# Kernel optimization log

Measured on AMD Instinct MI355X. Metric: run time of the kernel, lower is better.

The kernel has to match this reference:

```python
import jax, jax.numpy as jnp
import numpy as np

B, T, TC, C, CC, H = 2, 2048, 512, 1024, 512, 16
D = C // H  # head dim = 64


def setup_inputs() -> dict:
    key = jax.random.key(0)
    ks = jax.random.split(key, 18)
    w = lambda k, i, o: (jax.random.normal(k, (i, o), jnp.float32) / np.sqrt(i).astype(np.float32))
    return {
        "x": jax.random.normal(ks[0], (B, T, C), jnp.float32),
        "cross_input": jax.random.normal(ks[1], (B, TC, CC), jnp.float32),
        "Wk": w(ks[2], C, C),  "bk": jnp.zeros((C,), jnp.float32),
        "Wq": w(ks[3], C, C),  "bq": jnp.zeros((C,), jnp.float32),
        "Wv": w(ks[4], C, C),  "bv": jnp.zeros((C,), jnp.float32),
        "Wck": w(ks[5], CC, C), "bck": jnp.zeros((C,), jnp.float32),
        "Wcq": w(ks[6], C, C),  "bcq": jnp.zeros((C,), jnp.float32),
        "Wcv": w(ks[7], CC, C), "bcv": jnp.zeros((C,), jnp.float32),
        "Wp": w(ks[8], C, C),   "bp": jnp.zeros((C,), jnp.float32),
    }


def _heads(t):
    # [B, L, C] -> [B, H, L, D]
    b, l, _ = t.shape
    return t.reshape(b, l, H, D).transpose(0, 2, 1, 3)


def reference(x, cross_input, Wk, bk, Wq, bq, Wv, bv, Wck, bck, Wcq, bcq, Wcv, bcv, Wp, bp):
    scale = np.float32(1.0 / np.sqrt(D))
    q = _heads(x @ Wq + bq)
    k = _heads(x @ Wk + bk)
    v = _heads(x @ Wv + bv)
    # causal self-attention with materialized scores (faithful to original)
    att = jnp.einsum("bhqd,bhkd->bhqk", q, k) * scale
    causal = jnp.tril(jnp.ones((T, T), bool))
    att = jnp.where(causal[None, None], att, -jnp.inf)
    y = jnp.einsum("bhqk,bhkd->bhqd", jax.nn.softmax(att, axis=-1), v)
    # cross-attention (no mask)
    qc = _heads(x @ Wcq + bcq)
    kc = _heads(cross_input @ Wck + bck)
    vc = _heads(cross_input @ Wcv + bcv)
    attc = jnp.einsum("bhqd,bhkd->bhqk", qc, kc) * scale
    y = y + jnp.einsum("bhqk,bhkd->bhqd", jax.nn.softmax(attc, axis=-1), vc)
    # merge heads + output projection (dropout prob = 0 -> identity)
    y = y.transpose(0, 2, 1, 3).reshape(x.shape[0], T, C)
    return y @ Wp + bp
```

## Files before the change

### kernel.cpp

```cpp
#include <hip/hip_runtime.h>
#include <hip/hip_bf16.h>
#include <type_traits>

typedef __bf16 bf16;
typedef __bf16 bf16x8 __attribute__((ext_vector_type(8)));
typedef float floatx4 __attribute__((ext_vector_type(4)));
typedef unsigned int uint32x4 __attribute__((ext_vector_type(4)));

#if __has_builtin(__builtin_amdgcn_exp2f)
#define EXP2(x) __builtin_amdgcn_exp2f(x)
#else
#define EXP2(x) exp2f(x)
#endif

__device__ __forceinline__ void glds16(const bf16* g, bf16* l) {
  __builtin_amdgcn_global_load_lds((const __attribute__((address_space(1))) void*)g,
                                   (__attribute__((address_space(3))) void*)l, 16, 0, 0);
}

__device__ __forceinline__ unsigned pack_bf16(float a, float b) {
  unsigned short ua = __builtin_bit_cast(unsigned short, (bf16)a);
  unsigned short ub = __builtin_bit_cast(unsigned short, (bf16)b);
  return (unsigned)ua | ((unsigned)ub << 16);
}

struct PrepArgs {
  const float* x; const float* xc;
  bf16* xbf; bf16* xcbf;
  const float* b4[4];
  const float* bc[2];
  float* bias4; float* biasc;
  const float* W[7];
  bf16* WT[7];
};

__global__ __launch_bounds__(256) void prep_kernel(PrepArgs a) {
  __shared__ bf16 tsh[32][33];
  const int bx = blockIdx.x, tid = threadIdx.x;
  if (bx < 4096) {
    int i = bx * 256 + tid;
    float4 f = ((const float4*)a.x)[i];
    bf16 t[4] = {(bf16)f.x, (bf16)f.y, (bf16)f.z, (bf16)f.w};
    *(uint2*)&a.xbf[(long)i * 4] = *(const uint2*)t;
  } else if (bx < 4608) {
    int i = (bx - 4096) * 256 + tid;
    float4 f = ((const float4*)a.xc)[i];
    bf16 t[4] = {(bf16)f.x, (bf16)f.y, (bf16)f.z, (bf16)f.w};
    *(uint2*)&a.xcbf[(long)i * 4] = *(const uint2*)t;
  } else if (bx < 4632) {
    int lb = bx - 4608;
    if (lb < 16) {
      int i = lb * 256 + tid;
      int sec = i >> 10;
      float v = a.b4[sec][i & 1023];
      if (sec == 0 || sec == 3) v *= 0.18033688f;
      a.bias4[i] = v;
    } else {
      int i = (lb - 16) * 256 + tid;
      a.biasc[i] = a.bc[i >> 10][i & 1023];
    }
  } else {
    int t = bx - 4632, w, R, bxw, byw;
    if (t < 5120) { w = t >> 10; R = 1024; int l = t & 1023; bxw = l & 31; byw = l >> 5; }
    else { int t2 = t - 5120; w = 5 + (t2 >> 9); R = 512; int l = t2 & 511; bxw = l & 31; byw = l >> 5; }
    const float* in = a.W[w];
    bf16* out = a.WT[w];
    const float sc = (w == 0 || w == 3) ? 0.18033688f : 1.0f;
    int tx = tid & 31, ty = tid >> 5;
    int c = bxw * 32 + tx;
#pragma unroll
    for (int i = 0; i < 4; i++) {
      int r = byw * 32 + ty + i * 8;
      tsh[ty + i * 8][tx] = (bf16)(in[(long)r * 1024 + c] * sc);
    }
    __syncthreads();
    int oc = byw * 32 + tx;
#pragma unroll
    for (int i = 0; i < 4; i++) {
      int orr = bxw * 32 + ty + i * 8;
      out[(long)orr * R + oc] = tsh[tx][ty + i * 8];
    }
  }
}

template <typename OutT>
__global__ __launch_bounds__(256, 3) void gemm128(const bf16* __restrict__ A,
                                                  const bf16* __restrict__ Bt,
                                                  const float* __restrict__ bias,
                                                  OutT* __restrict__ C,
                                                  int M, int N, int K, int ldc,
                                                  bf16* __restrict__ Vt,
                                                  int vcol0, int vcol1, int Lt, int tok_shift) {
  __shared__ alignas(16) bf16 As[128 * 32];
  __shared__ alignas(16) bf16 Bs[128 * 32];
  const int tid = threadIdx.x, wave = tid >> 6, lane = tid & 63;
  const int l16 = lane & 15, l4 = lane >> 4;
  const int wm = wave & 1, wn = wave >> 1;
  const int n0 = blockIdx.x * 128, m0 = blockIdx.y * 128;
  const int lrow = lane >> 2, lch = (lane & 3) * 8;

  floatx4 acc[4][4];
#pragma unroll
  for (int mt = 0; mt < 4; mt++)
#pragma unroll
    for (int nt = 0; nt < 4; nt++) acc[mt][nt] = (floatx4){0.f, 0.f, 0.f, 0.f};

  const bf16* Ag = A + (long)(m0 + wave * 32 + lrow) * K + lch;
  const bf16* Bg = Bt + (long)(n0 + wave * 32 + lrow) * K + lch;
  bf16* Al = &As[(wave * 32) * 32];
  bf16* Bl = &Bs[(wave * 32) * 32];

  for (int k0 = 0; k0 < K; k0 += 32) {
    __syncthreads();
    glds16(Ag + k0, Al);
    glds16(Ag + k0 + (long)16 * K, Al + 16 * 32);
    glds16(Bg + k0, Bl);
    glds16(Bg + k0 + (long)16 * K, Bl + 16 * 32);
    __syncthreads();
    bf16x8 a[4], b[4];
#pragma unroll
    for (int mt = 0; mt < 4; mt++) a[mt] = *(const bf16x8*)&As[(wm * 64 + mt * 16 + l16) * 32 + l4 * 8];
#pragma unroll
    for (int nt = 0; nt < 4; nt++) b[nt] = *(const bf16x8*)&Bs[(wn * 64 + nt * 16 + l16) * 32 + l4 * 8];
#pragma unroll
    for (int mt = 0; mt < 4; mt++)
#pragma unroll
      for (int nt = 0; nt < 4; nt++)
        acc[mt][nt] = __builtin_amdgcn_mfma_f32_16x16x32_bf16(a[mt], b[nt], acc[mt][nt], 0, 0, 0);
  }

  const bool vpath = (vcol0 >= 0) && (n0 >= vcol0) && (n0 < vcol1);
  if (!vpath) {
    const int coladj = (vcol0 >= 0 && n0 >= vcol1) ? (vcol1 - vcol0) : 0;
#pragma unroll
    for (int nt = 0; nt < 4; nt++) {
      int col = n0 + wn * 64 + nt * 16 + l16;
      float bv = bias[col];
#pragma unroll
      for (int mt = 0; mt < 4; mt++)
#pragma unroll
        for (int r = 0; r < 4; r++) {
          int row = m0 + wm * 64 + mt * 16 + l4 * 4 + r;
          float v = acc[mt][nt][r] + bv;
          if constexpr (std::is_same_v<OutT, float>) C[(long)row * ldc + col - coladj] = v;
          else                                       C[(long)row * ldc + col - coladj] = (bf16)v;
        }
    }
  } else {
#pragma unroll
    for (int nt = 0; nt < 4; nt++) {
      int col = n0 + wn * 64 + nt * 16 + l16;
      int c = col - vcol0, hh = c >> 6, dd = c & 63;
      float bv = bias[col];
#pragma unroll
      for (int mt = 0; mt < 4; mt++) {
        int t0 = m0 + wm * 64 + mt * 16 + l4 * 4;
        int bb = t0 >> tok_shift, t = t0 & ((1 << tok_shift) - 1);
        t = (t & ~31) | (((t >> 2) & 3) << 3) | (((t >> 4) & 1) << 2) | (t & 3);
        bf16 tmp[4];
#pragma unroll
        for (int r = 0; r < 4; r++) tmp[r] = (bf16)(acc[mt][nt][r] + bv);
        *(uint2*)&Vt[(((long)bb * 16 + hh) * 64 + dd) * Lt + t] = *(const uint2*)tmp;
      }
    }
  }
}

__global__ __launch_bounds__(256, 2) void attn_kernel(const bf16* __restrict__ QKQc,
                                                      const bf16* __restrict__ VtB,
                                                      const bf16* __restrict__ KcB,
                                                      const bf16* __restrict__ VctB,
                                                      bf16* __restrict__ Y) {
  __shared__ float Lbuf[4][4][16];
  __shared__ alignas(16) bf16 U[4 * 64 * 72];
  const int tid = threadIdx.x, w = tid >> 6, lane = tid & 63;
  const int l16 = lane & 15, l4 = lane >> 4;
  const int bh = blockIdx.x, h = bh & 15, b = bh >> 4;
  const int qt = 31 - (int)blockIdx.y;
  const int q0 = qt * 64;
  const int wk = w * 32;
  const float NEG = -1e30f;

  float o_self[16];

  for (int phase = 0; phase < 2; phase++) {
    const bf16 *Qb, *Kb, *Vtb;
    int kstr, vtstr, nkt;
    if (phase == 0) {
      Qb = QKQc + (long)b * 2048 * 3072 + h * 64;
      Kb = Qb + 1024;                              kstr = 3072;
      Vtb = VtB + ((long)b * 16 + h) * 64 * 2048;  vtstr = 2048;
      nkt = (qt + 2) >> 1;
    } else {
      Qb = QKQc + (long)b * 2048 * 3072 + h * 64 + 2048;
      Kb = KcB + (long)b * 512 * 1024 + h * 64;    kstr = 1024;
      Vtb = VctB + ((long)b * 16 + h) * 64 * 512;  vtstr = 512;
      nkt = 4;
    }

    __syncthreads();

    bf16x8 qf[4][2];
#pragma unroll
    for (int qtt = 0; qtt < 4; qtt++) {
      const bf16* qp = Qb + (long)(q0 + qtt * 16 + l16) * 3072 + l4 * 8;
#pragma unroll
      for (int ds = 0; ds < 2; ds++) qf[qtt][ds] = *(const bf16x8*)(qp + ds * 32);
    }

    float l_i[4];
#pragma unroll
    for (int qtt = 0; qtt < 4; qtt++) l_i[qtt] = 0.f;
    floatx4 oacc[4][4];
#pragma unroll
    for (int mtd = 0; mtd < 4; mtd++)
#pragma unroll
      for (int qtt = 0; qtt < 4; qtt++) oacc[mtd][qtt] = (floatx4){0.f, 0.f, 0.f, 0.f};

    bf16x8 kreg[2][2];
#pragma unroll
    for (int mt = 0; mt < 2; mt++)
#pragma unroll
      for (int ds = 0; ds < 2; ds++)
        kreg[mt][ds] = *(const bf16x8*)(Kb + (long)(wk + mt * 16 + l16) * kstr + ds * 32 + l4 * 8);

    floatx4 sacc[2][4];
#pragma unroll
    for (int mt = 0; mt < 2; mt++)
#pragma unroll
      for (int qtt = 0; qtt < 4; qtt++) sacc[mt][qtt] = (floatx4){0.f, 0.f, 0.f, 0.f};
#pragma unroll
    for (int ds = 0; ds < 2; ds++)
#pragma unroll
      for (int mt = 0; mt < 2; mt++)
#pragma unroll
        for (int qtt = 0; qtt < 4; qtt++)
          sacc[mt][qtt] = __builtin_amdgcn_mfma_f32_16x16x32_bf16(kreg[mt][ds], qf[qtt][ds], sacc[mt][qtt], 0, 0, 0);

    for (int kt = 0; kt < nkt; kt++) {
      const int kbase = kt * 128 + wk;
      const bool more = (kt + 1 < nkt);

      bf16x8 vc[4];
#pragma unroll
      for (int mtd = 0; mtd < 4; mtd++)
        vc[mtd] = *(const bf16x8*)(Vtb + (long)(mtd * 16 + l16) * vtstr + kbase + l4 * 8);

      if (more) {
        const int nb = kbase + 128;
#pragma unroll
        for (int mt = 0; mt < 2; mt++)
#pragma unroll
          for (int ds = 0; ds < 2; ds++)
            kreg[mt][ds] = *(const bf16x8*)(Kb + (long)(nb + mt * 16 + l16) * kstr + ds * 32 + l4 * 8);
      }

      if (phase == 0 && kt == nkt - 1) {
#pragma unroll
        for (int mt = 0; mt < 2; mt++) {
          int keyb = kbase + mt * 16 + l4 * 4;
#pragma unroll
          for (int qtt = 0; qtt < 4; qtt++) {
            int q = q0 + qtt * 16 + l16;
#pragma unroll
            for (int r = 0; r < 4; r++)
              if (keyb + r > q) sacc[mt][qtt][r] = NEG;
          }
        }
      }

#pragma unroll
      for (int qtt = 0; qtt < 4; qtt++) {
        float p0 = EXP2(sacc[0][qtt][0]), p1 = EXP2(sacc[0][qtt][1]);
        float p2 = EXP2(sacc[0][qtt][2]), p3 = EXP2(sacc[0][qtt][3]);
        float p4 = EXP2(sacc[1][qtt][0]), p5 = EXP2(sacc[1][qtt][1]);
        float p6 = EXP2(sacc[1][qtt][2]), p7 = EXP2(sacc[1][qtt][3]);
        l_i[qtt] += ((p0 + p1) + (p2 + p3)) + ((p4 + p5) + (p6 + p7));
        uint32x4 pu = {pack_bf16(p0, p1), pack_bf16(p2, p3), pack_bf16(p4, p5), pack_bf16(p6, p7)};
        bf16x8 pf = __builtin_bit_cast(bf16x8, pu);
        __builtin_amdgcn_s_setprio(1);
#pragma unroll
        for (int mtd = 0; mtd < 4; mtd++)
          oacc[mtd][qtt] = __builtin_amdgcn_mfma_f32_16x16x32_bf16(vc[mtd], pf, oacc[mtd][qtt], 0, 0, 0);
        __builtin_amdgcn_s_setprio(0);
      }

      if (more) {
#pragma unroll
        for (int mt = 0; mt < 2; mt++)
#pragma unroll
          for (int qtt = 0; qtt < 4; qtt++) sacc[mt][qtt] = (floatx4){0.f, 0.f, 0.f, 0.f};
        __builtin_amdgcn_s_setprio(1);
#pragma unroll
        for (int ds = 0; ds < 2; ds++)
#pragma unroll
          for (int mt = 0; mt < 2; mt++)
#pragma unroll
            for (int qtt = 0; qtt < 4; qtt++)
              sacc[mt][qtt] = __builtin_amdgcn_mfma_f32_16x16x32_bf16(kreg[mt][ds], qf[qtt][ds], sacc[mt][qtt], 0, 0, 0);
        __builtin_amdgcn_s_setprio(0);
      }
    }

    float lsum[4];
#pragma unroll
    for (int qtt = 0; qtt < 4; qtt++) {
      float r = l_i[qtt];
      r += __shfl_xor(r, 16);
      r += __shfl_xor(r, 32);
      lsum[qtt] = r;
    }
    if (l4 == 0) {
#pragma unroll
      for (int qtt = 0; qtt < 4; qtt++) Lbuf[w][qtt][l16] = lsum[qtt];
    }
    __syncthreads();
    float denom[4];
#pragma unroll
    for (int qtt = 0; qtt < 4; qtt++)
      denom[qtt] = Lbuf[0][qtt][l16] + Lbuf[1][qtt][l16] + Lbuf[2][qtt][l16] + Lbuf[3][qtt][l16];
#pragma unroll
    for (int qtt = 0; qtt < 4; qtt++)
#pragma unroll
      for (int mtd = 0; mtd < 4; mtd++) {
        uint2 u = {pack_bf16(oacc[mtd][qtt][0], oacc[mtd][qtt][1]),
                   pack_bf16(oacc[mtd][qtt][2], oacc[mtd][qtt][3])};
        *(uint2*)&U[((w * 64) + qtt * 16 + l16) * 72 + mtd * 16 + l4 * 4] = u;
      }
    __syncthreads();
    float sum[16];
#pragma unroll
    for (int j = 0; j < 16; j++) sum[j] = 0.f;
#pragma unroll
    for (int s = 0; s < 4; s++) {
      bf16x8 c0 = *(const bf16x8*)&U[((s * 64) + w * 16 + l16) * 72 + l4 * 16];
      bf16x8 c1 = *(const bf16x8*)&U[((s * 64) + w * 16 + l16) * 72 + l4 * 16 + 8];
#pragma unroll
      for (int j = 0; j < 8; j++) { sum[j] += (float)c0[j]; sum[8 + j] += (float)c1[j]; }
    }
    float invd = 1.0f / denom[w];
    if (phase == 0) {
#pragma unroll
      for (int j = 0; j < 16; j++) o_self[j] = sum[j] * invd;
    } else {
      long row = (long)b * 2048 + q0 + w * 16 + l16;
      bf16 out[16];
#pragma unroll
      for (int j = 0; j < 16; j++) out[j] = (bf16)(o_self[j] + sum[j] * invd);
      *(bf16x8*)&Y[row * 1024 + h * 64 + l4 * 16] = *(const bf16x8*)&out[0];
      *(bf16x8*)&Y[row * 1024 + h * 64 + l4 * 16 + 8] = *(const bf16x8*)&out[8];
    }
  }
}

extern "C" void kernel_launch(void* const* d_in, const int* in_sizes, int n_in,
                              void* d_out, int out_size, void* d_ws, size_t ws_size,
                              hipStream_t stream) {
  const float* x   = (const float*)d_in[0];
  const float* xc  = (const float*)d_in[1];
  const float* Wk  = (const float*)d_in[2];  const float* bk  = (const float*)d_in[3];
  const float* Wq  = (const float*)d_in[4];  const float* bq  = (const float*)d_in[5];
  const float* Wv  = (const float*)d_in[6];  const float* bv  = (const float*)d_in[7];
  const float* Wck = (const float*)d_in[8];  const float* bck = (const float*)d_in[9];
  const float* Wcq = (const float*)d_in[10]; const float* bcq = (const float*)d_in[11];
  const float* Wcv = (const float*)d_in[12]; const float* bcv = (const float*)d_in[13];
  const float* Wp  = (const float*)d_in[14]; const float* bp  = (const float*)d_in[15];

  char* ws = (char*)d_ws;
  const size_t MB = 1ull << 20;
  bf16*  WT_all = (bf16*)(ws + 0);
  bf16*  WC_all = (bf16*)(ws + 8 * MB);
  bf16*  WpT    = (bf16*)(ws + 10 * MB);
  bf16*  xbf    = (bf16*)(ws + 12 * MB);
  bf16*  Yb     = xbf;
  bf16*  xcbf   = (bf16*)(ws + 20 * MB);
  float* bias4  = (float*)(ws + 21 * MB);
  float* biasc  = (float*)(ws + 21 * MB + 65536);
  bf16*  QKQc   = (bf16*)(ws + 22 * MB);
  bf16*  VtB    = (bf16*)(ws + 46 * MB);
  bf16*  KcB    = (bf16*)(ws + 54 * MB);
  bf16*  VctB   = (bf16*)(ws + 56 * MB);

  PrepArgs pa;
  pa.x = x; pa.xc = xc; pa.xbf = xbf; pa.xcbf = xcbf;
  pa.b4[0] = bq; pa.b4[1] = bk; pa.b4[2] = bv; pa.b4[3] = bcq;
  pa.bc[0] = bck; pa.bc[1] = bcv;
  pa.bias4 = bias4; pa.biasc = biasc;
  pa.W[0] = Wq;  pa.WT[0] = WT_all + 0ll * 1024 * 1024;
  pa.W[1] = Wk;  pa.WT[1] = WT_all + 1ll * 1024 * 1024;
  pa.W[2] = Wv;  pa.WT[2] = WT_all + 2ll * 1024 * 1024;
  pa.W[3] = Wcq; pa.WT[3] = WT_all + 3ll * 1024 * 1024;
  pa.W[4] = Wp;  pa.WT[4] = WpT;
  pa.W[5] = Wck; pa.WT[5] = WC_all + 0ll * 1024 * 512;
  pa.W[6] = Wcv; pa.WT[6] = WC_all + 1ll * 1024 * 512;
  prep_kernel<<<10776, 256, 0, stream>>>(pa);

  gemm128<bf16><<<dim3(32, 32), 256, 0, stream>>>(xbf, WT_all, bias4, QKQc,
                                                  4096, 4096, 1024, 3072,
                                                  VtB, 2048, 3072, 2048, 11);
  gemm128<bf16><<<dim3(16, 8), 256, 0, stream>>>(xcbf, WC_all, biasc, KcB,
                                                 1024, 2048, 512, 1024,
                                                 VctB, 1024, 2048, 512, 9);

  attn_kernel<<<dim3(32, 32), 256, 0, stream>>>(QKQc, VtB, KcB, VctB, Yb);

  gemm128<float><<<dim3(8, 32), 256, 0, stream>>>(Yb, WpT, bp, (float*)d_out,
                                                  4096, 1024, 1024, 1024,
                                                  nullptr, -1, -1, 0, 0);
}
```

Before: 262.3 us.

## Double-buffer K/V register prefetch in attention loop and spill self output to LDS

Restructures the attention key-tile loop into a two-way ping-pong over register buffers, so V is prefetched two tiles ahead and K three tiles ahead instead of loading V at the start of each iteration. The phase-0 self-attention output is moved from registers into an LDS buffer to lower register pressure and make room for the extra prefetch buffers. The denominator read is also simplified to a single per-wave value. The deeper prefetch adds registers and LDS use, which could reduce occupancy below the two-blocks-per-CU launch bound.

```diff
diff --git a/kernel.cpp b/kernel.cpp
--- a/kernel.cpp
+++ b/kernel.cpp
@@ -173,6 +173,7 @@
                                                       bf16* __restrict__ Y) {
   __shared__ float Lbuf[4][4][16];
   __shared__ alignas(16) bf16 U[4 * 64 * 72];
+  __shared__ alignas(16) float Osave[256][20];
   const int tid = threadIdx.x, w = tid >> 6, lane = tid & 63;
   const int l16 = lane & 15, l4 = lane >> 4;
   const int bh = blockIdx.x, h = bh & 15, b = bh >> 4;
@@ -180,8 +181,6 @@
   const int q0 = qt * 64;
   const int wk = w * 32;
   const float NEG = -1e30f;
-
-  float o_self[16];
 
   for (int phase = 0; phase < 2; phase++) {
     const bf16 *Qb, *Kb, *Vtb;
@@ -217,44 +216,51 @@
 #pragma unroll
       for (int qtt = 0; qtt < 4; qtt++) oacc[mtd][qtt] = (floatx4){0.f, 0.f, 0.f, 0.f};
 
-    bf16x8 kreg[2][2];
-#pragma unroll
-    for (int mt = 0; mt < 2; mt++)
+    floatx4 sacc[2][4];
+    bf16x8 vA[4], vB[4], kA[2][2], kB[2][2];
+
+    {
+      bf16x8 k0[2][2];
+#pragma unroll
+      for (int mt = 0; mt < 2; mt++)
+#pragma unroll
+        for (int ds = 0; ds < 2; ds++)
+          k0[mt][ds] = *(const bf16x8*)(Kb + (long)(wk + mt * 16 + l16) * kstr + ds * 32 + l4 * 8);
+#pragma unroll
+      for (int mtd = 0; mtd < 4; mtd++)
+        vA[mtd] = *(const bf16x8*)(Vtb + (long)(mtd * 16 + l16) * vtstr + wk + l4 * 8);
+      if (nkt > 1) {
+#pragma unroll
+        for (int mt = 0; mt < 2; mt++)
+#pragma unroll
+          for (int ds = 0; ds < 2; ds++)
+            kA[mt][ds] = *(const bf16x8*)(Kb + (long)(128 + wk + mt * 16 + l16) * kstr + ds * 32 + l4 * 8);
+#pragma unroll
+        for (int mtd = 0; mtd < 4; mtd++)
+          vB[mtd] = *(const bf16x8*)(Vtb + (long)(mtd * 16 + l16) * vtstr + 128 + wk + l4 * 8);
+      }
+      if (nkt > 2) {
+#pragma unroll
+        for (int mt = 0; mt < 2; mt++)
+#pragma unroll
+          for (int ds = 0; ds < 2; ds++)
+            kB[mt][ds] = *(const bf16x8*)(Kb + (long)(256 + wk + mt * 16 + l16) * kstr + ds * 32 + l4 * 8);
+      }
+#pragma unroll
+      for (int mt = 0; mt < 2; mt++)
+#pragma unroll
+        for (int qtt = 0; qtt < 4; qtt++) sacc[mt][qtt] = (floatx4){0.f, 0.f, 0.f, 0.f};
 #pragma unroll
       for (int ds = 0; ds < 2; ds++)
-        kreg[mt][ds] = *(const bf16x8*)(Kb + (long)(wk + mt * 16 + l16) * kstr + ds * 32 + l4 * 8);
-
-    floatx4 sacc[2][4];
-#pragma unroll
-    for (int mt = 0; mt < 2; mt++)
-#pragma unroll
-      for (int qtt = 0; qtt < 4; qtt++) sacc[mt][qtt] = (floatx4){0.f, 0.f, 0.f, 0.f};
-#pragma unroll
-    for (int ds = 0; ds < 2; ds++)
-#pragma unroll
-      for (int mt = 0; mt < 2; mt++)
-#pragma unroll
-        for (int qtt = 0; qtt < 4; qtt++)
-          sacc[mt][qtt] = __builtin_amdgcn_mfma_f32_16x16x32_bf16(kreg[mt][ds], qf[qtt][ds], sacc[mt][qtt], 0, 0, 0);
-
-    for (int kt = 0; kt < nkt; kt++) {
+#pragma unroll
+        for (int mt = 0; mt < 2; mt++)
+#pragma unroll
+          for (int qtt = 0; qtt < 4; qtt++)
+            sacc[mt][qtt] = __builtin_amdgcn_mfma_f32_16x16x32_bf16(k0[mt][ds], qf[qtt][ds], sacc[mt][qtt], 0, 0, 0);
+    }
+
+    auto body = [&](bf16x8 (&vX)[4], bf16x8 (&kX)[2][2], int kt) {
       const int kbase = kt * 128 + wk;
-      const bool more = (kt + 1 < nkt);
-
-      bf16x8 vc[4];
-#pragma unroll
-      for (int mtd = 0; mtd < 4; mtd++)
-        vc[mtd] = *(const bf16x8*)(Vtb + (long)(mtd * 16 + l16) * vtstr + kbase + l4 * 8);
-
-      if (more) {
-        const int nb = kbase + 128;
-#pragma unroll
-        for (int mt = 0; mt < 2; mt++)
-#pragma unroll
-          for (int ds = 0; ds < 2; ds++)
-            kreg[mt][ds] = *(const bf16x8*)(Kb + (long)(nb + mt * 16 + l16) * kstr + ds * 32 + l4 * 8);
-      }
-
       if (phase == 0 && kt == nkt - 1) {
 #pragma unroll
         for (int mt = 0; mt < 2; mt++) {
@@ -268,7 +274,6 @@
           }
         }
       }
-
 #pragma unroll
       for (int qtt = 0; qtt < 4; qtt++) {
         float p0 = EXP2(sacc[0][qtt][0]), p1 = EXP2(sacc[0][qtt][1]);
@@ -281,11 +286,16 @@
         __builtin_amdgcn_s_setprio(1);
 #pragma unroll
         for (int mtd = 0; mtd < 4; mtd++)
-          oacc[mtd][qtt] = __builtin_amdgcn_mfma_f32_16x16x32_bf16(vc[mtd], pf, oacc[mtd][qtt], 0, 0, 0);
+          oacc[mtd][qtt] = __builtin_amdgcn_mfma_f32_16x16x32_bf16(vX[mtd], pf, oacc[mtd][qtt], 0, 0, 0);
         __builtin_amdgcn_s_setprio(0);
       }
-
-      if (more) {
+      if (kt + 2 < nkt) {
+        const int nb = kbase + 256;
+#pragma unroll
+        for (int mtd = 0; mtd < 4; mtd++)
+          vX[mtd] = *(const bf16x8*)(Vtb + (long)(mtd * 16 + l16) * vtstr + nb + l4 * 8);
+      }
+      if (kt + 1 < nkt) {
 #pragma unroll
         for (int mt = 0; mt < 2; mt++)
 #pragma unroll
@@ -297,9 +307,25 @@
           for (int mt = 0; mt < 2; mt++)
 #pragma unroll
             for (int qtt = 0; qtt < 4; qtt++)
-              sacc[mt][qtt] = __builtin_amdgcn_mfma_f32_16x16x32_bf16(kreg[mt][ds], qf[qtt][ds], sacc[mt][qtt], 0, 0, 0);
+              sacc[mt][qtt] = __builtin_amdgcn_mfma_f32_16x16x32_bf16(kX[mt][ds], qf[qtt][ds], sacc[mt][qtt], 0, 0, 0);
         __builtin_amdgcn_s_setprio(0);
       }
+      if (kt + 3 < nkt) {
+        const int nb = kbase + 384;
+#pragma unroll
+        for (int mt = 0; mt < 2; mt++)
+#pragma unroll
+          for (int ds = 0; ds < 2; ds++)
+            kX[mt][ds] = *(const bf16x8*)(Kb + (long)(nb + mt * 16 + l16) * kstr + ds * 32 + l4 * 8);
+      }
+    };
+
+    int kt = 0;
+    while (true) {
+      body(vA, kA, kt);
+      if (++kt == nkt) break;
+      body(vB, kB, kt);
+      if (++kt == nkt) break;
     }
 
     float lsum[4];
@@ -315,10 +341,9 @@
       for (int qtt = 0; qtt < 4; qtt++) Lbuf[w][qtt][l16] = lsum[qtt];
     }
     __syncthreads();
-    float denom[4];
-#pragma unroll
-    for (int qtt = 0; qtt < 4; qtt++)
-      denom[qtt] = Lbuf[0][qtt][l16] + Lbuf[1][qtt][l16] + Lbuf[2][qtt][l16] + Lbuf[3][qtt][l16];
+    float denom = 0.f;
+#pragma unroll
+    for (int s = 0; s < 4; s++) denom += Lbuf[s][w][l16];
 #pragma unroll
     for (int qtt = 0; qtt < 4; qtt++)
 #pragma unroll
@@ -338,15 +363,25 @@
 #pragma unroll
       for (int j = 0; j < 8; j++) { sum[j] += (float)c0[j]; sum[8 + j] += (float)c1[j]; }
     }
-    float invd = 1.0f / denom[w];
+    float invd = 1.0f / denom;
     if (phase == 0) {
 #pragma unroll
-      for (int j = 0; j < 16; j++) o_self[j] = sum[j] * invd;
+      for (int jj = 0; jj < 4; jj++) {
+        float4 v = {sum[jj * 4] * invd, sum[jj * 4 + 1] * invd,
+                    sum[jj * 4 + 2] * invd, sum[jj * 4 + 3] * invd};
+        *(float4*)&Osave[tid][jj * 4] = v;
+      }
     } else {
       long row = (long)b * 2048 + q0 + w * 16 + l16;
       bf16 out[16];
 #pragma unroll
-      for (int j = 0; j < 16; j++) out[j] = (bf16)(o_self[j] + sum[j] * invd);
+      for (int jj = 0; jj < 4; jj++) {
+        float4 v = *(const float4*)&Osave[tid][jj * 4];
+        out[jj * 4]     = (bf16)(v.x + sum[jj * 4] * invd);
+        out[jj * 4 + 1] = (bf16)(v.y + sum[jj * 4 + 1] * invd);
+        out[jj * 4 + 2] = (bf16)(v.z + sum[jj * 4 + 2] * invd);
+        out[jj * 4 + 3] = (bf16)(v.w + sum[jj * 4 + 3] * invd);
+      }
       *(bf16x8*)&Y[row * 1024 + h * 64 + l4 * 16] = *(const bf16x8*)&out[0];
       *(bf16x8*)&Y[row * 1024 + h * 64 + l4 * 16 + 8] = *(const bf16x8*)&out[8];
     }
```

Result: slower. 271.6 us (+3.5%).
